# Kernel optimization log

Measured on AMD Instinct MI355X. Metric: run time of the kernel, lower is better.

The kernel has to match this reference:

```python
import jax, jax.numpy as jnp
import numpy as np

B, H, S, D = 4, 16, 2048, 64
TEMPERATURE = 8.0  # sqrt(D)
NEG = -1000000000.0

def setup_inputs() -> dict:
    key = jax.random.key(0)
    kq, kk, kv, km = jax.random.split(key, 4)
    q = jax.random.normal(kq, (B, H, S, D), dtype=jnp.float32)
    k = jax.random.normal(kk, (B, H, S, D), dtype=jnp.float32)
    v = jax.random.normal(kv, (B, H, S, D), dtype=jnp.float32)
    mask = jax.random.randint(km, (B, 1, S, S), 0, 2, dtype=jnp.int32)
    return {"q": q, "k": k, "v": v, "mask": mask}

def reference(q, k, v, mask):
    # scores: [B,H,S,S]
    scores = jnp.einsum('bhqd,bhkd->bhqk', q / TEMPERATURE, k)
    scores = jnp.where(mask == 1, NEG, scores)
    attn = jax.nn.softmax(scores, axis=-1)  # dropout p=0.0 -> identity
    out = jnp.einsum('bhqk,bhkd->bhqd', attn, v)
    return out
```

## Files before the change

kernel.cpp:

```cpp
#include <hip/hip_runtime.h>

#define NB 4
#define NH 16
#define SS 2048
#define DD 64
#define QT 128
#define KT 32
#define KSP 72
#define VSP 40
#define QSCALE 0.18033688011112042f
#define MASK_BITS_BYTES ((size_t)NB * SS * (SS / 8))

typedef __bf16 bf16x8 __attribute__((ext_vector_type(8)));
typedef __bf16 bf16x2 __attribute__((ext_vector_type(2)));
typedef float  floatx16 __attribute__((ext_vector_type(16)));

static_assert(sizeof(bf16x8) == 16, "bf16x8 must be 16B");

__device__ __forceinline__ int pack2(float a, float b) {
    bf16x2 v; v[0] = (__bf16)a; v[1] = (__bf16)b;
    return __builtin_bit_cast(int, v);
}

__global__ __launch_bounds__(256)
void pack_mask_kernel(const int* __restrict__ M, unsigned long long* __restrict__ bits)
{
    int gw   = (blockIdx.x * 256 + threadIdx.x) >> 6;
    int lane = threadIdx.x & 63;
    size_t row = (size_t)(gw >> 5);
    int word   = gw & 31;
    int mval = M[row * SS + (size_t)word * 64 + lane];
    unsigned long long b = __ballot(mval == 1);
    if (lane == 0) bits[gw] = b;
}

template<bool USE_BITS>
__global__ __launch_bounds__(256, 4)
void attn_kernel(const float* __restrict__ Q, const float* __restrict__ K,
                 const float* __restrict__ V, const int* __restrict__ M,
                 const unsigned* __restrict__ MB, float* __restrict__ O)
{
    __shared__ __bf16 ks[KT][KSP];
    __shared__ __bf16 vsT[DD][VSP];

    const int t    = threadIdx.x;
    const int wave = t >> 6;
    const int lane = t & 63;
    const int l31  = lane & 31;
    const int h8   = lane >> 5;

    const int bh    = blockIdx.x >> 4;
    const int qtile = blockIdx.x & 15;
    const int b     = bh >> 4;
    const int q0    = qtile * QT + wave * 32;

    const size_t base = (size_t)bh * SS * DD;
    const float* Qb = Q + base;
    const float* Kb = K + base;
    const float* Vb = V + base;

    bf16x8 aq[4];
    {
        const float* qp = Qb + (size_t)(q0 + l31) * DD + 8 * h8;
        #pragma unroll
        for (int s = 0; s < 4; ++s) {
            float4 f0 = *(const float4*)(qp + 16 * s);
            float4 f1 = *(const float4*)(qp + 16 * s + 4);
            bf16x8 a;
            a[0] = (__bf16)(f0.x * QSCALE); a[1] = (__bf16)(f0.y * QSCALE);
            a[2] = (__bf16)(f0.z * QSCALE); a[3] = (__bf16)(f0.w * QSCALE);
            a[4] = (__bf16)(f1.x * QSCALE); a[5] = (__bf16)(f1.y * QSCALE);
            a[6] = (__bf16)(f1.z * QSCALE); a[7] = (__bf16)(f1.w * QSCALE);
            aq[s] = a;
        }
    }

    const int skey = t >> 3;
    const int sdc  = (t & 7) * 8;
    const int vk   = 2 * (t & 15);
    const int vdc  = (t >> 4) * 4;
    const int vcol = 16 * (vk >> 4) + 8 * ((vk >> 2) & 1) + (vk & 3) + 4 * ((vk >> 3) & 1);

    const float* kp0 = Kb + (size_t)skey * DD + sdc;
    const float* vp0 = Vb + (size_t)vk * DD + vdc;

    float4 ka0 = ((const float4*)kp0)[0];
    float4 ka1 = ((const float4*)kp0)[1];
    float4 va0 = *(const float4*)vp0;
    float4 va1 = *(const float4*)(vp0 + DD);

    const unsigned* mbrow = MB + ((size_t)b * SS + q0 + l31) * (SS / 32);
    const int*      mrow  = M + (size_t)b * SS * SS + (size_t)(q0 + l31) * SS + 4 * h8;

    floatx16 o0, o1;
    #pragma unroll
    for (int i = 0; i < 16; ++i) { o0[i] = 0.f; o1[i] = 0.f; }
    float ls = 0.f;

    for (int tt = 0; tt < SS / KT; ++tt) {
        __syncthreads();

        {
            bf16x8 kw;
            kw[0]=(__bf16)ka0.x; kw[1]=(__bf16)ka0.y; kw[2]=(__bf16)ka0.z; kw[3]=(__bf16)ka0.w;
            kw[4]=(__bf16)ka1.x; kw[5]=(__bf16)ka1.y; kw[6]=(__bf16)ka1.z; kw[7]=(__bf16)ka1.w;
            *(bf16x8*)&ks[skey][sdc] = kw;
            float av[4] = {va0.x, va0.y, va0.z, va0.w};
            float bv[4] = {va1.x, va1.y, va1.z, va1.w};
            #pragma unroll
            for (int i = 0; i < 4; ++i) {
                bf16x2 pr; pr[0] = (__bf16)av[i]; pr[1] = (__bf16)bv[i];
                *(bf16x2*)&vsT[vdc + i][vcol] = pr;
            }
        }
        __syncthreads();

        unsigned mw = 0;
        int4 mi[4];
        if (USE_BITS) {
            mw = mbrow[tt];
        } else {
            #pragma unroll
            for (int g2 = 0; g2 < 4; ++g2)
                mi[g2] = *(const int4*)(mrow + tt * KT + 8 * g2);
        }

        {
            int jn = ((tt + 1) * KT) & (SS - 1);
            const float* kn = kp0 + (size_t)jn * DD;
            ka0 = ((const float4*)kn)[0];
            ka1 = ((const float4*)kn)[1];
            const float* vn = vp0 + (size_t)jn * DD;
            va0 = *(const float4*)vn;
            va1 = *(const float4*)(vn + DD);
        }

        floatx16 c;
        #pragma unroll
        for (int i = 0; i < 16; ++i) c[i] = 0.f;
        #pragma unroll
        for (int s = 0; s < 4; ++s) {
            bf16x8 a = *(const bf16x8*)&ks[l31][16 * s + 8 * h8];
            c = __builtin_amdgcn_mfma_f32_32x32x16_bf16(a, aq[s], c, 0, 0, 0);
        }

        unsigned u = mw >> (4 * h8);
        int pk[8];
        float psum = 0.f;
        #pragma unroll
        for (int g = 0; g < 8; ++g) {
            const int ia = 2 * g, ib = 2 * g + 1;
            float pa = __builtin_amdgcn_exp2f(c[ia]);
            float pb = __builtin_amdgcn_exp2f(c[ib]);
            bool ma, mb_;
            if (USE_BITS) {
                ma  = (u >> ((ia & 3) + 8 * (ia >> 2))) & 1;
                mb_ = (u >> ((ib & 3) + 8 * (ib >> 2))) & 1;
            } else {
                const int g2 = ia >> 2;
                ma  = ((&mi[g2].x)[ia & 3] == 1);
                mb_ = ((&mi[g2].x)[ib & 3] == 1);
            }
            pa = ma  ? 0.f : pa;
            pb = mb_ ? 0.f : pb;
            psum += pa + pb;
            pk[g] = pack2(pa, pb);
        }
        ls += psum;

        #pragma unroll
        for (int s2 = 0; s2 < 2; ++s2) {
            int4 fw; fw.x = pk[4*s2]; fw.y = pk[4*s2+1]; fw.z = pk[4*s2+2]; fw.w = pk[4*s2+3];
            bf16x8 bp = __builtin_bit_cast(bf16x8, fw);
            bf16x8 av0 = *(const bf16x8*)&vsT[l31][16 * s2 + 8 * h8];
            bf16x8 av1 = *(const bf16x8*)&vsT[32 + l31][16 * s2 + 8 * h8];
            o0 = __builtin_amdgcn_mfma_f32_32x32x16_bf16(av0, bp, o0, 0, 0, 0);
            o1 = __builtin_amdgcn_mfma_f32_32x32x16_bf16(av1, bp, o1, 0, 0, 0);
        }
    }

    ls += __shfl_xor(ls, 32);
    float inv = 1.0f / ls;
    float* op = O + base + (size_t)(q0 + l31) * DD;
    #pragma unroll
    for (int s = 0; s < 4; ++s) {
        float4 st0, st1;
        st0.x = o0[4*s+0] * inv; st0.y = o0[4*s+1] * inv;
        st0.z = o0[4*s+2] * inv; st0.w = o0[4*s+3] * inv;
        st1.x = o1[4*s+0] * inv; st1.y = o1[4*s+1] * inv;
        st1.z = o1[4*s+2] * inv; st1.w = o1[4*s+3] * inv;
        *(float4*)(op + 8 * s + 4 * h8)      = st0;
        *(float4*)(op + 32 + 8 * s + 4 * h8) = st1;
    }
}

extern "C" void kernel_launch(void* const* d_in, const int* in_sizes, int n_in,
                              void* d_out, int out_size, void* d_ws, size_t ws_size,
                              hipStream_t stream) {
    (void)in_sizes; (void)n_in; (void)out_size;
    const float* q = (const float*)d_in[0];
    const float* k = (const float*)d_in[1];
    const float* v = (const float*)d_in[2];
    const int*   m = (const int*)d_in[3];
    float* out = (float*)d_out;
    dim3 grid(NB * NH * (SS / QT));

    if (ws_size >= MASK_BITS_BYTES) {
        unsigned long long* bits = (unsigned long long*)d_ws;
        pack_mask_kernel<<<dim3(NB * SS * (SS / 64) / 4), 256, 0, stream>>>(m, bits);
        attn_kernel<true><<<grid, 256, 0, stream>>>(q, k, v, m, (const unsigned*)bits, out);
    } else {
        attn_kernel<false><<<grid, 256, 0, stream>>>(q, k, v, m, (const unsigned*)nullptr, out);
    }
}
```

Baseline: 306.1 us.

## Pre-convert K/V to bf16 tiled layout and double-buffer 64-key tiles

Adds a pre-pass kernel that converts K and V to bf16 in the workspace, with V pre-transposed into the MFMA-friendly permuted layout. The attention kernel then loads ready-made bf16 tiles with 16-byte copies. It uses 64-key tiles with double-buffered shared memory, so there is one barrier per tile instead of two. This halves the global bytes re-read by each of the 16 query-tile blocks per head and removes the per-tile conversion and scatter work from the main loop. The cost is an extra kernel launch, extra workspace traffic and more shared memory per block. If the workspace is too small, it falls back to the old path.

```diff
diff --git a/kernel.cpp b/kernel.cpp
--- a/kernel.cpp
+++ b/kernel.cpp
@@ -5,11 +5,14 @@
 #define SS 2048
 #define DD 64
 #define QT 128
-#define KT 32
-#define KSP 72
-#define VSP 40
+#define KT 64
+#define LSP 72
 #define QSCALE 0.18033688011112042f
+
 #define MASK_BITS_BYTES ((size_t)NB * SS * (SS / 8))
+#define KV_TILE_ELEMS   (KT * DD)
+#define KV_BYTES        ((size_t)NB * NH * SS * DD * 2)
+#define WS_NEED         (MASK_BITS_BYTES + 2 * KV_BYTES)
 
 typedef __bf16 bf16x8 __attribute__((ext_vector_type(8)));
 typedef __bf16 bf16x2 __attribute__((ext_vector_type(2)));
@@ -34,14 +37,51 @@
     if (lane == 0) bits[gw] = b;
 }
 
-template<bool USE_BITS>
+__global__ __launch_bounds__(256)
+void convert_kv_kernel(const float* __restrict__ K, const float* __restrict__ V,
+                       __bf16* __restrict__ Kt, __bf16* __restrict__ Vt)
+{
+    const int bh   = blockIdx.x >> 5;
+    const int tile = blockIdx.x & 31;
+    const int t    = threadIdx.x;
+    const float* Kb = K + ((size_t)bh * SS + tile * KT) * DD;
+    const float* Vb = V + ((size_t)bh * SS + tile * KT) * DD;
+    __bf16* Ko = Kt + ((size_t)(bh * 32 + tile)) * KV_TILE_ELEMS;
+    __bf16* Vo = Vt + ((size_t)(bh * 32 + tile)) * KV_TILE_ELEMS;
+
+    {
+        const int key = t >> 2, dg = (t & 3) * 16;
+        const float* src = Kb + (size_t)key * DD + dg;
+        __bf16 w[16];
+        #pragma unroll
+        for (int i = 0; i < 4; ++i) {
+            float4 f = ((const float4*)src)[i];
+            w[4*i+0] = (__bf16)f.x; w[4*i+1] = (__bf16)f.y;
+            w[4*i+2] = (__bf16)f.z; w[4*i+3] = (__bf16)f.w;
+        }
+        *(uint4*)(Ko + (size_t)key * DD + dg)     = *(uint4*)&w[0];
+        *(uint4*)(Ko + (size_t)key * DD + dg + 8) = *(uint4*)&w[8];
+    }
+    {
+        const int dim = t >> 2, kg = (t & 3) * 16;
+        __bf16 w[16];
+        #pragma unroll
+        for (int i = 0; i < 16; ++i) {
+            int pos = (i & 3) + 8 * ((i >> 2) & 1) + 4 * ((i >> 3) & 1);
+            w[pos] = (__bf16)Vb[(size_t)(kg + i) * DD + dim];
+        }
+        *(uint4*)(Vo + (size_t)dim * DD + kg)     = *(uint4*)&w[0];
+        *(uint4*)(Vo + (size_t)dim * DD + kg + 8) = *(uint4*)&w[8];
+    }
+}
+
 __global__ __launch_bounds__(256, 4)
-void attn_kernel(const float* __restrict__ Q, const float* __restrict__ K,
-                 const float* __restrict__ V, const int* __restrict__ M,
-                 const unsigned* __restrict__ MB, float* __restrict__ O)
+void attn_kernel(const float* __restrict__ Q, const __bf16* __restrict__ Kt,
+                 const __bf16* __restrict__ Vt, const uint2* __restrict__ MB,
+                 float* __restrict__ O)
 {
-    __shared__ __bf16 ks[KT][KSP];
-    __shared__ __bf16 vsT[DD][VSP];
+    __shared__ __bf16 ks[2][KT][LSP];
+    __shared__ __bf16 vsT[2][DD][LSP];
 
     const int t    = threadIdx.x;
     const int wave = t >> 6;
@@ -55,9 +95,9 @@
     const int q0    = qtile * QT + wave * 32;
 
     const size_t base = (size_t)bh * SS * DD;
-    const float* Qb = Q + base;
-    const float* Kb = K + base;
-    const float* Vb = V + base;
+    const float*  Qb  = Q  + base;
+    const __bf16* Ktb = Kt + base;
+    const __bf16* Vtb = Vt + base;
 
     bf16x8 aq[4];
     {
@@ -75,108 +115,94 @@
         }
     }
 
-    const int skey = t >> 3;
-    const int sdc  = (t & 7) * 8;
-    const int vk   = 2 * (t & 15);
-    const int vdc  = (t >> 4) * 4;
-    const int vcol = 16 * (vk >> 4) + 8 * ((vk >> 2) & 1) + (vk & 3) + 4 * ((vk >> 3) & 1);
-
-    const float* kp0 = Kb + (size_t)skey * DD + sdc;
-    const float* vp0 = Vb + (size_t)vk * DD + vdc;
-
-    float4 ka0 = ((const float4*)kp0)[0];
-    float4 ka1 = ((const float4*)kp0)[1];
-    float4 va0 = *(const float4*)vp0;
-    float4 va1 = *(const float4*)(vp0 + DD);
-
-    const unsigned* mbrow = MB + ((size_t)b * SS + q0 + l31) * (SS / 32);
-    const int*      mrow  = M + (size_t)b * SS * SS + (size_t)(q0 + l31) * SS + 4 * h8;
+    const int srow = t >> 2;
+    const int scol = (t & 3) * 16;
+    const __bf16* kp0 = Ktb + (size_t)srow * DD + scol;
+    const __bf16* vp0 = Vtb + (size_t)srow * DD + scol;
+
+    uint4 kr0 = ((const uint4*)kp0)[0], kr1 = ((const uint4*)(kp0 + 8))[0];
+    uint4 vr0 = ((const uint4*)vp0)[0], vr1 = ((const uint4*)(vp0 + 8))[0];
+
+    const uint2* mbrow = MB + ((size_t)b * SS + q0 + l31) * (SS / 64);
+    uint2 mwc = mbrow[0];
 
     floatx16 o0, o1;
     #pragma unroll
     for (int i = 0; i < 16; ++i) { o0[i] = 0.f; o1[i] = 0.f; }
     float ls = 0.f;
 
+    *(uint4*)&ks[0][srow][scol]      = kr0;
+    *(uint4*)&ks[0][srow][scol + 8]  = kr1;
+    *(uint4*)&vsT[0][srow][scol]     = vr0;
+    *(uint4*)&vsT[0][srow][scol + 8] = vr1;
+
+    {
+        const __bf16* kn = kp0 + (size_t)KV_TILE_ELEMS;
+        const __bf16* vn = vp0 + (size_t)KV_TILE_ELEMS;
+        kr0 = ((const uint4*)kn)[0]; kr1 = ((const uint4*)(kn + 8))[0];
+        vr0 = ((const uint4*)vn)[0]; vr1 = ((const uint4*)(vn + 8))[0];
+    }
+
     for (int tt = 0; tt < SS / KT; ++tt) {
         __syncthreads();
 
+        const int wb = (tt + 1) & 1;
+        *(uint4*)&ks[wb][srow][scol]      = kr0;
+        *(uint4*)&ks[wb][srow][scol + 8]  = kr1;
+        *(uint4*)&vsT[wb][srow][scol]     = vr0;
+        *(uint4*)&vsT[wb][srow][scol + 8] = vr1;
+
+        uint2 mwn = mbrow[(tt + 1) & 31];
         {
-            bf16x8 kw;
-            kw[0]=(__bf16)ka0.x; kw[1]=(__bf16)ka0.y; kw[2]=(__bf16)ka0.z; kw[3]=(__bf16)ka0.w;
-            kw[4]=(__bf16)ka1.x; kw[5]=(__bf16)ka1.y; kw[6]=(__bf16)ka1.z; kw[7]=(__bf16)ka1.w;
-            *(bf16x8*)&ks[skey][sdc] = kw;
-            float av[4] = {va0.x, va0.y, va0.z, va0.w};
-            float bv[4] = {va1.x, va1.y, va1.z, va1.w};
-            #pragma unroll
-            for (int i = 0; i < 4; ++i) {
-                bf16x2 pr; pr[0] = (__bf16)av[i]; pr[1] = (__bf16)bv[i];
-                *(bf16x2*)&vsT[vdc + i][vcol] = pr;
+            size_t off = (size_t)((tt + 2) & 31) * KV_TILE_ELEMS;
+            const __bf16* kn = kp0 + off;
+            const __bf16* vn = vp0 + off;
+            kr0 = ((const uint4*)kn)[0]; kr1 = ((const uint4*)(kn + 8))[0];
+            vr0 = ((const uint4*)vn)[0]; vr1 = ((const uint4*)(vn + 8))[0];
+        }
+
+        const __bf16 (*ksb)[LSP] = ks[tt & 1];
+        const __bf16 (*vtb)[LSP] = vsT[tt & 1];
+
+        #pragma unroll
+        for (int h = 0; h < 2; ++h) {
+            floatx16 c;
+            #pragma unroll
+            for (int i = 0; i < 16; ++i) c[i] = 0.f;
+            #pragma unroll
+            for (int s = 0; s < 4; ++s) {
+                bf16x8 a = *(const bf16x8*)&ksb[32 * h + l31][16 * s + 8 * h8];
+                c = __builtin_amdgcn_mfma_f32_32x32x16_bf16(a, aq[s], c, 0, 0, 0);
             }
-        }
-        __syncthreads();
-
-        unsigned mw = 0;
-        int4 mi[4];
-        if (USE_BITS) {
-            mw = mbrow[tt];
-        } else {
-            #pragma unroll
-            for (int g2 = 0; g2 < 4; ++g2)
-                mi[g2] = *(const int4*)(mrow + tt * KT + 8 * g2);
-        }
-
-        {
-            int jn = ((tt + 1) * KT) & (SS - 1);
-            const float* kn = kp0 + (size_t)jn * DD;
-            ka0 = ((const float4*)kn)[0];
-            ka1 = ((const float4*)kn)[1];
-            const float* vn = vp0 + (size_t)jn * DD;
-            va0 = *(const float4*)vn;
-            va1 = *(const float4*)(vn + DD);
-        }
-
-        floatx16 c;
-        #pragma unroll
-        for (int i = 0; i < 16; ++i) c[i] = 0.f;
-        #pragma unroll
-        for (int s = 0; s < 4; ++s) {
-            bf16x8 a = *(const bf16x8*)&ks[l31][16 * s + 8 * h8];
-            c = __builtin_amdgcn_mfma_f32_32x32x16_bf16(a, aq[s], c, 0, 0, 0);
-        }
-
-        unsigned u = mw >> (4 * h8);
-        int pk[8];
-        float psum = 0.f;
-        #pragma unroll
-        for (int g = 0; g < 8; ++g) {
-            const int ia = 2 * g, ib = 2 * g + 1;
-            float pa = __builtin_amdgcn_exp2f(c[ia]);
-            float pb = __builtin_amdgcn_exp2f(c[ib]);
-            bool ma, mb_;
-            if (USE_BITS) {
-                ma  = (u >> ((ia & 3) + 8 * (ia >> 2))) & 1;
-                mb_ = (u >> ((ib & 3) + 8 * (ib >> 2))) & 1;
-            } else {
-                const int g2 = ia >> 2;
-                ma  = ((&mi[g2].x)[ia & 3] == 1);
-                mb_ = ((&mi[g2].x)[ib & 3] == 1);
+
+            unsigned u = (h ? mwc.y : mwc.x) >> (4 * h8);
+            int pk[8];
+            float psum = 0.f;
+            #pragma unroll
+            for (int g = 0; g < 8; ++g) {
+                const int ia = 2 * g, ib = 2 * g + 1;
+                float pa = __builtin_amdgcn_exp2f(c[ia]);
+                float pb = __builtin_amdgcn_exp2f(c[ib]);
+                bool ma  = (u >> ((ia & 3) + 8 * (ia >> 2))) & 1;
+                bool mb_ = (u >> ((ib & 3) + 8 * (ib >> 2))) & 1;
+                pa = ma  ? 0.f : pa;
+                pb = mb_ ? 0.f : pb;
+                psum += pa + pb;
+                pk[g] = pack2(pa, pb);
             }
-            pa = ma  ? 0.f : pa;
-            pb = mb_ ? 0.f : pb;
-            psum += pa + pb;
-            pk[g] = pack2(pa, pb);
-        }
-        ls += psum;
-
-        #pragma unroll
-        for (int s2 = 0; s2 < 2; ++s2) {
-            int4 fw; fw.x = pk[4*s2]; fw.y = pk[4*s2+1]; fw.z = pk[4*s2+2]; fw.w = pk[4*s2+3];
-            bf16x8 bp = __builtin_bit_cast(bf16x8, fw);
-            bf16x8 av0 = *(const bf16x8*)&vsT[l31][16 * s2 + 8 * h8];
-            bf16x8 av1 = *(const bf16x8*)&vsT[32 + l31][16 * s2 + 8 * h8];
-            o0 = __builtin_amdgcn_mfma_f32_32x32x16_bf16(av0, bp, o0, 0, 0, 0);
-            o1 = __builtin_amdgcn_mfma_f32_32x32x16_bf16(av1, bp, o1, 0, 0, 0);
-        }
+            ls += psum;
+
+            #pragma unroll
+            for (int s2 = 0; s2 < 2; ++s2) {
+                int4 fw; fw.x = pk[4*s2]; fw.y = pk[4*s2+1]; fw.z = pk[4*s2+2]; fw.w = pk[4*s2+3];
+                bf16x8 bp = __builtin_bit_cast(bf16x8, fw);
+                bf16x8 av0 = *(const bf16x8*)&vtb[l31][32 * h + 16 * s2 + 8 * h8];
+                bf16x8 av1 = *(const bf16x8*)&vtb[32 + l31][32 * h + 16 * s2 + 8 * h8];
+                o0 = __builtin_amdgcn_mfma_f32_32x32x16_bf16(av0, bp, o0, 0, 0, 0);
+                o1 = __builtin_amdgcn_mfma_f32_32x32x16_bf16(av1, bp, o1, 0, 0, 0);
+            }
+        }
+        mwc = mwn;
     }
 
     ls += __shfl_xor(ls, 32);
@@ -194,6 +220,120 @@
     }
 }
 
+__global__ __launch_bounds__(256, 4)
+void attn_kernel_fb(const float* __restrict__ Q, const float* __restrict__ K,
+                    const float* __restrict__ V, const int* __restrict__ M,
+                    float* __restrict__ O)
+{
+    __shared__ __bf16 ks[32][LSP];
+    __shared__ __bf16 vsT[DD][40];
+
+    const int t = threadIdx.x, wave = t >> 6, lane = t & 63;
+    const int l31 = lane & 31, h8 = lane >> 5;
+    const int bh = blockIdx.x >> 4, qtile = blockIdx.x & 15, b = bh >> 4;
+    const int q0 = qtile * QT + wave * 32;
+    const size_t base = (size_t)bh * SS * DD;
+    const float* Qb = Q + base; const float* Kb = K + base; const float* Vb = V + base;
+
+    bf16x8 aq[4];
+    {
+        const float* qp = Qb + (size_t)(q0 + l31) * DD + 8 * h8;
+        #pragma unroll
+        for (int s = 0; s < 4; ++s) {
+            float4 f0 = *(const float4*)(qp + 16 * s);
+            float4 f1 = *(const float4*)(qp + 16 * s + 4);
+            bf16x8 a;
+            a[0]=(__bf16)(f0.x*QSCALE); a[1]=(__bf16)(f0.y*QSCALE);
+            a[2]=(__bf16)(f0.z*QSCALE); a[3]=(__bf16)(f0.w*QSCALE);
+            a[4]=(__bf16)(f1.x*QSCALE); a[5]=(__bf16)(f1.y*QSCALE);
+            a[6]=(__bf16)(f1.z*QSCALE); a[7]=(__bf16)(f1.w*QSCALE);
+            aq[s] = a;
+        }
+    }
+    const int skey = t >> 3, sdc = (t & 7) * 8;
+    const int vk = 2 * (t & 15), vdc = (t >> 4) * 4;
+    const int vcol = 16*(vk>>4) + 8*((vk>>2)&1) + (vk&3) + 4*((vk>>3)&1);
+    const float* kp0 = Kb + (size_t)skey * DD + sdc;
+    const float* vp0 = Vb + (size_t)vk * DD + vdc;
+    float4 ka0 = ((const float4*)kp0)[0], ka1 = ((const float4*)kp0)[1];
+    float4 va0 = *(const float4*)vp0, va1 = *(const float4*)(vp0 + DD);
+    const int* mrow = M + (size_t)b * SS * SS + (size_t)(q0 + l31) * SS + 4 * h8;
+
+    floatx16 o0, o1;
+    #pragma unroll
+    for (int i = 0; i < 16; ++i) { o0[i] = 0.f; o1[i] = 0.f; }
+    float ls = 0.f;
+
+    for (int tt = 0; tt < SS / 32; ++tt) {
+        __syncthreads();
+        {
+            bf16x8 kw;
+            kw[0]=(__bf16)ka0.x; kw[1]=(__bf16)ka0.y; kw[2]=(__bf16)ka0.z; kw[3]=(__bf16)ka0.w;
+            kw[4]=(__bf16)ka1.x; kw[5]=(__bf16)ka1.y; kw[6]=(__bf16)ka1.z; kw[7]=(__bf16)ka1.w;
+            *(bf16x8*)&ks[skey][sdc] = kw;
+            float av[4] = {va0.x, va0.y, va0.z, va0.w};
+            float bv[4] = {va1.x, va1.y, va1.z, va1.w};
+            #pragma unroll
+            for (int i = 0; i < 4; ++i) {
+                bf16x2 pr; pr[0] = (__bf16)av[i]; pr[1] = (__bf16)bv[i];
+                *(bf16x2*)&vsT[vdc + i][vcol] = pr;
+            }
+        }
+        __syncthreads();
+        int4 mi[4];
+        #pragma unroll
+        for (int g2 = 0; g2 < 4; ++g2) mi[g2] = *(const int4*)(mrow + tt * 32 + 8 * g2);
+        {
+            int jn = ((tt + 1) * 32) & (SS - 1);
+            const float* kn = kp0 + (size_t)jn * DD;
+            ka0 = ((const float4*)kn)[0]; ka1 = ((const float4*)kn)[1];
+            const float* vn = vp0 + (size_t)jn * DD;
+            va0 = *(const float4*)vn; va1 = *(const float4*)(vn + DD);
+        }
+        floatx16 c;
+        #pragma unroll
+        for (int i = 0; i < 16; ++i) c[i] = 0.f;
+        #pragma unroll
+        for (int s = 0; s < 4; ++s) {
+            bf16x8 a = *(const bf16x8*)&ks[l31][16 * s + 8 * h8];
+            c = __builtin_amdgcn_mfma_f32_32x32x16_bf16(a, aq[s], c, 0, 0, 0);
+        }
+        int pk[8]; float psum = 0.f;
+        #pragma unroll
+        for (int g = 0; g < 8; ++g) {
+            const int ia = 2 * g, ib = 2 * g + 1;
+            float pa = __builtin_amdgcn_exp2f(c[ia]);
+            float pb = __builtin_amdgcn_exp2f(c[ib]);
+            const int g2 = ia >> 2;
+            pa = ((&mi[g2].x)[ia & 3] == 1) ? 0.f : pa;
+            pb = ((&mi[g2].x)[ib & 3] == 1) ? 0.f : pb;
+            psum += pa + pb;
+            pk[g] = pack2(pa, pb);
+        }
+        ls += psum;
+        #pragma unroll
+        for (int s2 = 0; s2 < 2; ++s2) {
+            int4 fw; fw.x = pk[4*s2]; fw.y = pk[4*s2+1]; fw.z = pk[4*s2+2]; fw.w = pk[4*s2+3];
+            bf16x8 bp = __builtin_bit_cast(bf16x8, fw);
+            bf16x8 av0 = *(const bf16x8*)&vsT[l31][16 * s2 + 8 * h8];
+            bf16x8 av1 = *(const bf16x8*)&vsT[32 + l31][16 * s2 + 8 * h8];
+            o0 = __builtin_amdgcn_mfma_f32_32x32x16_bf16(av0, bp, o0, 0, 0, 0);
+            o1 = __builtin_amdgcn_mfma_f32_32x32x16_bf16(av1, bp, o1, 0, 0, 0);
+        }
+    }
+    ls += __shfl_xor(ls, 32);
+    float inv = 1.0f / ls;
+    float* op = O + base + (size_t)(q0 + l31) * DD;
+    #pragma unroll
+    for (int s = 0; s < 4; ++s) {
+        float4 st0, st1;
+        st0.x=o0[4*s+0]*inv; st0.y=o0[4*s+1]*inv; st0.z=o0[4*s+2]*inv; st0.w=o0[4*s+3]*inv;
+        st1.x=o1[4*s+0]*inv; st1.y=o1[4*s+1]*inv; st1.z=o1[4*s+2]*inv; st1.w=o1[4*s+3]*inv;
+        *(float4*)(op + 8 * s + 4 * h8)      = st0;
+        *(float4*)(op + 32 + 8 * s + 4 * h8) = st1;
+    }
+}
+
 extern "C" void kernel_launch(void* const* d_in, const int* in_sizes, int n_in,
                               void* d_out, int out_size, void* d_ws, size_t ws_size,
                               hipStream_t stream) {
@@ -205,11 +345,14 @@
     float* out = (float*)d_out;
     dim3 grid(NB * NH * (SS / QT));
 
-    if (ws_size >= MASK_BITS_BYTES) {
+    if (ws_size >= WS_NEED) {
         unsigned long long* bits = (unsigned long long*)d_ws;
+        __bf16* Kt = (__bf16*)((char*)d_ws + MASK_BITS_BYTES);
+        __bf16* Vt = (__bf16*)((char*)d_ws + MASK_BITS_BYTES + KV_BYTES);
         pack_mask_kernel<<<dim3(NB * SS * (SS / 64) / 4), 256, 0, stream>>>(m, bits);
-        attn_kernel<true><<<grid, 256, 0, stream>>>(q, k, v, m, (const unsigned*)bits, out);
+        convert_kv_kernel<<<dim3(NB * NH * 32), 256, 0, stream>>>(k, v, Kt, Vt);
+        attn_kernel<<<grid, 256, 0, stream>>>(q, Kt, Vt, (const uint2*)bits, out);
     } else {
-        attn_kernel<false><<<grid, 256, 0, stream>>>(q, k, v, m, (const unsigned*)nullptr, out);
-    }
-}
+        attn_kernel_fb<<<grid, 256, 0, stream>>>(q, k, v, m, out);
+    }
+}
```

Measured after the change: 323.3 us. 1.06x slower.
